# Kernel optimization log

Hardware: AMD Instinct MI355X
Metric: run time of the kernel (lower is better)

Reference implementation:

```python
import jax, jax.numpy as jnp
import numpy as np
import math

SCALE = 64.0
MARGIN = 0.5
THRESH = math.cos(math.pi - MARGIN)          # cos(pi - m)
MM = math.sin(math.pi - MARGIN) * MARGIN     # sin(pi - m) * m
N, D, C = 512, 512, 100000


def setup_inputs() -> dict:
    key = jax.random.key(0)
    k1, k2, k3 = jax.random.split(key, 3)
    x = jax.random.normal(k1, (N, D), dtype=jnp.float32)
    label = jax.random.randint(k2, (N,), 0, C, dtype=jnp.int64)
    # reset_parameters: uniform(-stdv, stdv), stdv = 1/sqrt(in_features)
    stdv = 1.0 / math.sqrt(D)
    weight = jax.random.uniform(k3, (C, D), dtype=jnp.float32, minval=-stdv, maxval=stdv)
    return {"input": x, "label": label, "weight": weight}


def reference(input, label, weight):
    # row-wise L2 normalize features and class weights
    ex = input / jnp.linalg.norm(input, axis=1, keepdims=True)
    ew = weight / jnp.linalg.norm(weight, axis=1, keepdims=True)
    cos = jnp.einsum("nd,cd->nc", ex, ew)               # [N, C]
    rows = jnp.arange(cos.shape[0])
    cos_l = cos[rows, label]                              # cos at the label column
    cond = cos_l > THRESH                                 # easy-margin condition per row
    onehot = (jnp.arange(cos.shape[1])[None, :] == label[:, None])
    a = jnp.where(onehot & cond[:, None], MARGIN, 0.0).astype(cos.dtype)
    b = jnp.where(onehot & (~cond[:, None]), -MM, 0.0).astype(cos.dtype)
    # clamp slightly inside [-1,1] to guard acos against fp roundoff
    cos_c = jnp.clip(cos, -1.0 + 1e-7, 1.0 - 1e-7)
    logits = SCALE * (jnp.cos(jnp.arccos(cos_c) + a) + b)
    return logits
```

## Files before the change

kernel.cpp:

```cpp
#include <hip/hip_runtime.h>
#include <hip/hip_bf16.h>
#include <stdint.h>


#define NROWS 512
#define DDIM 512
#define NCLS 100000
#define NCLS_PAD 100096

typedef __attribute__((ext_vector_type(8))) short bf16x8;
typedef __attribute__((ext_vector_type(4))) float f32x4;

__device__ __forceinline__ unsigned short f2bf(float x) {
    union { float f; uint32_t u; } c; c.f = x;
    uint32_t r = (c.u + 0x7FFFu + ((c.u >> 16) & 1u)) >> 16;
    return (unsigned short)r;
}

__device__ __forceinline__ void g2lds16(const void* g, void* l) {
    __builtin_amdgcn_global_load_lds(
        (const __attribute__((address_space(1))) void*)g,
        (__attribute__((address_space(3))) void*)l, 16, 0, 0);
}

__global__ __launch_bounds__(256)
void rownorm_all(const float* __restrict__ x, const float* __restrict__ w,
                 unsigned short* __restrict__ Abf, unsigned short* __restrict__ Wbf) {
    const int wv   = threadIdx.x >> 6;
    const int lane = threadIdx.x & 63;

    const float* in;
    unsigned short* orow;
    int validRows, row;
    if (blockIdx.x < 128) {
        row = blockIdx.x * 4 + wv;
        in = x; orow = Abf + (size_t)row * DDIM; validRows = NROWS;
    } else {
        row = (blockIdx.x - 128) * 4 + wv;
        in = w; orow = Wbf + (size_t)row * DDIM; validRows = NCLS;
    }

    if (row >= validRows) {
        ushort4 z = {0, 0, 0, 0};
        *(ushort4*)(orow + lane * 4) = z;
        *(ushort4*)(orow + 256 + lane * 4) = z;
        return;
    }

    const float4* p = (const float4*)(in + (size_t)row * DDIM);
    float4 v0 = p[lane];
    float4 v1 = p[64 + lane];

    float ss = v0.x*v0.x + v0.y*v0.y + v0.z*v0.z + v0.w*v0.w
             + v1.x*v1.x + v1.y*v1.y + v1.z*v1.z + v1.w*v1.w;
    #pragma unroll
    for (int off = 32; off > 0; off >>= 1) ss += __shfl_xor(ss, off);
    const float r = rsqrtf(ss);

    ushort4 o0, o1;
    o0.x = f2bf(v0.x * r); o0.y = f2bf(v0.y * r);
    o0.z = f2bf(v0.z * r); o0.w = f2bf(v0.w * r);
    o1.x = f2bf(v1.x * r); o1.y = f2bf(v1.y * r);
    o1.z = f2bf(v1.z * r); o1.w = f2bf(v1.w * r);
    *(ushort4*)(orow + lane * 4) = o0;
    *(ushort4*)(orow + 256 + lane * 4) = o1;
}

__global__ __launch_bounds__(256)
void arcface_gemm(const unsigned short* __restrict__ A,
                  const unsigned short* __restrict__ B,
                  float* __restrict__ out) {
    __shared__ unsigned short As[128 * 32];
    __shared__ unsigned short Bs[128 * 32];

    const int bid = blockIdx.x;
    int panel, slot;
    if (bid < 3104) { panel = (bid >> 5) * 8 + (bid & 7); slot = (bid >> 3) & 3; }
    else            { int l = bid - 3104; panel = 776 + l % 6; slot = l / 6; }
    const int rowBase = slot * 128;
    const int colBase = panel * 128;

    const int t    = threadIdx.x;
    const int lane = t & 63;
    const int wid  = t >> 6;
    const int wr   = wid >> 1;
    const int wc   = wid & 1;

    f32x4 acc[4][4] = {};

    const unsigned short* gA = A + (size_t)(rowBase + (t >> 2)) * DDIM + ((t & 3) << 3);
    const unsigned short* gB = B + (size_t)(colBase + (t >> 2)) * DDIM + ((t & 3) << 3);

    const int kg = (lane >> 4) << 3;
    const int fr = lane & 15;

    for (int kt = 0; kt < DDIM; kt += 32) {
        __syncthreads();
        g2lds16(gA + kt,             &As[t * 8]);
        g2lds16(gA + kt + 64 * DDIM, &As[2048 + t * 8]);
        g2lds16(gB + kt,             &Bs[t * 8]);
        g2lds16(gB + kt + 64 * DDIM, &Bs[2048 + t * 8]);
        __syncthreads();

        bf16x8 a[4], b[4];
        #pragma unroll
        for (int m = 0; m < 4; ++m)
            a[m] = *(const bf16x8*)&As[(wr * 64 + m * 16 + fr) * 32 + kg];
        #pragma unroll
        for (int n = 0; n < 4; ++n)
            b[n] = *(const bf16x8*)&Bs[(wc * 64 + n * 16 + fr) * 32 + kg];

        #pragma unroll
        for (int m = 0; m < 4; ++m)
            #pragma unroll
            for (int n = 0; n < 4; ++n)
                acc[m][n] = __builtin_amdgcn_mfma_f32_16x16x32_bf16(
                    a[m], b[n], acc[m][n], 0, 0, 0);
    }

    const float lo = -1.0f + 1e-7f, hi = 1.0f - 1e-7f;
    #pragma unroll
    for (int m = 0; m < 4; ++m) {
        const int r = rowBase + wr * 64 + m * 16 + ((lane >> 4) << 2);
        #pragma unroll
        for (int n = 0; n < 4; ++n) {
            const int c = colBase + wc * 64 + n * 16 + fr;
            if (c < NCLS) {
                #pragma unroll
                for (int i = 0; i < 4; ++i) {
                    float v = acc[m][n][i];
                    v = fminf(fmaxf(v, lo), hi);
                    out[(size_t)(r + i) * NCLS + c] = 64.0f * v;
                }
            }
        }
    }
}

__global__ void arcface_fixup(const int* __restrict__ label, float* __restrict__ out) {
    const int n = blockIdx.x * 64 + threadIdx.x;
    if (n >= NROWS) return;
    const int c = label[n];
    const size_t idx = (size_t)n * NCLS + c;
    const float t = out[idx] * 0.015625f;
    const float COSM = 0.8775825618903728f;
    const float SINM = 0.479425538604203f;
    const float MM   = 0.2397127693021015f;
    const float THRESH = -0.8775825618903728f;
    float r;
    if (t > THRESH) {
        r = t * COSM - sqrtf(fmaxf(1.0f - t * t, 0.0f)) * SINM;
    } else {
        r = t - MM;
    }
    out[idx] = 64.0f * r;
}

extern "C" void kernel_launch(void* const* d_in, const int* in_sizes, int n_in,
                              void* d_out, int out_size, void* d_ws, size_t ws_size,
                              hipStream_t stream) {
    const float* x     = (const float*)d_in[0];
    const int*   label = (const int*)d_in[1];
    const float* w     = (const float*)d_in[2];
    float* out = (float*)d_out;

    unsigned short* Abf = (unsigned short*)d_ws;
    unsigned short* Wbf = (unsigned short*)d_ws + (size_t)NROWS * DDIM;

    rownorm_all<<<128 + NCLS_PAD / 4, 256, 0, stream>>>(x, w, Abf, Wbf);

    arcface_gemm<<<3128, 256, 0, stream>>>(Abf, Wbf, out);

    arcface_fixup<<<(NROWS + 63) / 64, 64, 0, stream>>>(label, out);
}
```

Baseline: 429.4 us.

## Fuse weight normalization and margin fixup into double-buffered GEMM

```diff
diff --git a/kernel.cpp b/kernel.cpp
--- a/kernel.cpp
+++ b/kernel.cpp
@@ -6,9 +6,9 @@
 #define NROWS 512
 #define DDIM 512
 #define NCLS 100000
-#define NCLS_PAD 100096
 
 typedef __attribute__((ext_vector_type(8))) short bf16x8;
+typedef __attribute__((ext_vector_type(8))) unsigned short u16x8;
 typedef __attribute__((ext_vector_type(4))) float f32x4;
 
 __device__ __forceinline__ unsigned short f2bf(float x) {
@@ -24,28 +24,9 @@
 }
 
 __global__ __launch_bounds__(256)
-void rownorm_all(const float* __restrict__ x, const float* __restrict__ w,
-                 unsigned short* __restrict__ Abf, unsigned short* __restrict__ Wbf) {
-    const int wv   = threadIdx.x >> 6;
+void rownorm_x(const float* __restrict__ in, unsigned short* __restrict__ out) {
+    const int row  = blockIdx.x * 4 + (threadIdx.x >> 6);
     const int lane = threadIdx.x & 63;
-
-    const float* in;
-    unsigned short* orow;
-    int validRows, row;
-    if (blockIdx.x < 128) {
-        row = blockIdx.x * 4 + wv;
-        in = x; orow = Abf + (size_t)row * DDIM; validRows = NROWS;
-    } else {
-        row = (blockIdx.x - 128) * 4 + wv;
-        in = w; orow = Wbf + (size_t)row * DDIM; validRows = NCLS;
-    }
-
-    if (row >= validRows) {
-        ushort4 z = {0, 0, 0, 0};
-        *(ushort4*)(orow + lane * 4) = z;
-        *(ushort4*)(orow + 256 + lane * 4) = z;
-        return;
-    }
 
     const float4* p = (const float4*)(in + (size_t)row * DDIM);
     float4 v0 = p[lane];
@@ -57,6 +38,7 @@
     for (int off = 32; off > 0; off >>= 1) ss += __shfl_xor(ss, off);
     const float r = rsqrtf(ss);
 
+    unsigned short* orow = out + (size_t)row * DDIM;
     ushort4 o0, o1;
     o0.x = f2bf(v0.x * r); o0.y = f2bf(v0.y * r);
     o0.z = f2bf(v0.z * r); o0.w = f2bf(v0.w * r);
@@ -67,11 +49,14 @@
 }
 
 __global__ __launch_bounds__(256)
-void arcface_gemm(const unsigned short* __restrict__ A,
-                  const unsigned short* __restrict__ B,
-                  float* __restrict__ out) {
-    __shared__ unsigned short As[128 * 32];
-    __shared__ unsigned short Bs[128 * 32];
+void arcface_gemm_fused(const unsigned short* __restrict__ A,
+                        const float* __restrict__ W,
+                        const int* __restrict__ labels,
+                        float* __restrict__ out) {
+    __shared__ unsigned short As[2][128 * 32];
+    __shared__ unsigned short Bs[2][128 * 40];
+    __shared__ float ssp[128];
+    __shared__ int   lab_s[128];
 
     const int bid = blockIdx.x;
     int panel, slot;
@@ -85,30 +70,78 @@
     const int wid  = t >> 6;
     const int wr   = wid >> 1;
     const int wc   = wid & 1;
-
+    const int kg   = (lane >> 4) << 3;
+    const int fr   = lane & 15;
+
+    if (t < 128) lab_s[t] = labels[rowBase + t];
+
+    const int brow = t >> 1;
+    const int kc   = (t & 1) << 4;
+    const int cls  = colBase + brow;
+    const bool bv  = cls < NCLS;
+    const float* gB = W + (size_t)(bv ? cls : 0) * DDIM + kc;
+    unsigned short* wB[2] = { &Bs[0][brow * 40 + kc], &Bs[1][brow * 40 + kc] };
+
+    const unsigned short* gA = A + (size_t)(rowBase + (t >> 2)) * DDIM + ((t & 3) << 3);
+
+    float ss = 0.f;
     f32x4 acc[4][4] = {};
 
-    const unsigned short* gA = A + (size_t)(rowBase + (t >> 2)) * DDIM + ((t & 3) << 3);
-    const unsigned short* gB = B + (size_t)(colBase + (t >> 2)) * DDIM + ((t & 3) << 3);
-
-    const int kg = (lane >> 4) << 3;
-    const int fr = lane & 15;
-
-    for (int kt = 0; kt < DDIM; kt += 32) {
-        __syncthreads();
-        g2lds16(gA + kt,             &As[t * 8]);
-        g2lds16(gA + kt + 64 * DDIM, &As[2048 + t * 8]);
-        g2lds16(gB + kt,             &Bs[t * 8]);
-        g2lds16(gB + kt + 64 * DDIM, &Bs[2048 + t * 8]);
-        __syncthreads();
+    float4 p0, p1, p2, p3;
+    g2lds16(gA,             &As[0][t * 8]);
+    g2lds16(gA + 64 * DDIM, &As[0][2048 + t * 8]);
+    if (bv) {
+        p0 = *(const float4*)(gB + 0);  p1 = *(const float4*)(gB + 4);
+        p2 = *(const float4*)(gB + 8);  p3 = *(const float4*)(gB + 12);
+    } else {
+        p0 = float4{0,0,0,0}; p1 = p0; p2 = p0; p3 = p0;
+    }
+
+    #pragma unroll
+    for (int tt = 0; tt < 16; ++tt) {
+        const int cur = tt & 1;
+
+        __builtin_amdgcn_s_barrier();
+        __builtin_amdgcn_sched_barrier(0);
+        asm volatile("s_waitcnt vmcnt(0)" ::: "memory");
+        __builtin_amdgcn_sched_barrier(0);
+
+        ss += p0.x*p0.x + p0.y*p0.y + p0.z*p0.z + p0.w*p0.w;
+        ss += p1.x*p1.x + p1.y*p1.y + p1.z*p1.z + p1.w*p1.w;
+        ss += p2.x*p2.x + p2.y*p2.y + p2.z*p2.z + p2.w*p2.w;
+        ss += p3.x*p3.x + p3.y*p3.y + p3.z*p3.z + p3.w*p3.w;
+        u16x8 o0, o1;
+        o0[0]=f2bf(p0.x); o0[1]=f2bf(p0.y); o0[2]=f2bf(p0.z); o0[3]=f2bf(p0.w);
+        o0[4]=f2bf(p1.x); o0[5]=f2bf(p1.y); o0[6]=f2bf(p1.z); o0[7]=f2bf(p1.w);
+        o1[0]=f2bf(p2.x); o1[1]=f2bf(p2.y); o1[2]=f2bf(p2.z); o1[3]=f2bf(p2.w);
+        o1[4]=f2bf(p3.x); o1[5]=f2bf(p3.y); o1[6]=f2bf(p3.z); o1[7]=f2bf(p3.w);
+        *(u16x8*)(wB[cur])     = o0;
+        *(u16x8*)(wB[cur] + 8) = o1;
+
+        if (tt < 15) {
+            const int kt = (tt + 1) * 32;
+            g2lds16(gA + kt,             &As[cur ^ 1][t * 8]);
+            g2lds16(gA + kt + 64 * DDIM, &As[cur ^ 1][2048 + t * 8]);
+            if (bv) {
+                p0 = *(const float4*)(gB + kt + 0);
+                p1 = *(const float4*)(gB + kt + 4);
+                p2 = *(const float4*)(gB + kt + 8);
+                p3 = *(const float4*)(gB + kt + 12);
+            }
+        }
+
+        asm volatile("s_waitcnt lgkmcnt(0)" ::: "memory");
+        __builtin_amdgcn_sched_barrier(0);
+        __builtin_amdgcn_s_barrier();
+        __builtin_amdgcn_sched_barrier(0);
 
         bf16x8 a[4], b[4];
         #pragma unroll
         for (int m = 0; m < 4; ++m)
-            a[m] = *(const bf16x8*)&As[(wr * 64 + m * 16 + fr) * 32 + kg];
+            a[m] = *(const bf16x8*)&As[cur][(wr * 64 + m * 16 + fr) * 32 + kg];
         #pragma unroll
         for (int n = 0; n < 4; ++n)
-            b[n] = *(const bf16x8*)&Bs[(wc * 64 + n * 16 + fr) * 32 + kg];
+            b[n] = *(const bf16x8*)&Bs[cur][(wc * 64 + n * 16 + fr) * 40 + kg];
 
         #pragma unroll
         for (int m = 0; m < 4; ++m)
@@ -118,42 +151,43 @@
                     a[m], b[n], acc[m][n], 0, 0, 0);
     }
 
+    float sst = ss + __shfl_xor(ss, 1);
+    if ((t & 1) == 0) ssp[t >> 1] = sst;
+    __syncthreads();
+
     const float lo = -1.0f + 1e-7f, hi = 1.0f - 1e-7f;
+    const float COSM = 0.8775825618903728f;
+    const float SINM = 0.479425538604203f;
+    const float MM   = 0.2397127693021015f;
+    const float THR  = -0.8775825618903728f;
+
+    float rn[4];
+    #pragma unroll
+    for (int n = 0; n < 4; ++n)
+        rn[n] = rsqrtf(ssp[wc * 64 + n * 16 + fr]);
+
     #pragma unroll
     for (int m = 0; m < 4; ++m) {
-        const int r = rowBase + wr * 64 + m * 16 + ((lane >> 4) << 2);
+        const int rloc = wr * 64 + m * 16 + ((lane >> 4) << 2);
         #pragma unroll
         for (int n = 0; n < 4; ++n) {
             const int c = colBase + wc * 64 + n * 16 + fr;
             if (c < NCLS) {
                 #pragma unroll
                 for (int i = 0; i < 4; ++i) {
-                    float v = acc[m][n][i];
-                    v = fminf(fmaxf(v, lo), hi);
-                    out[(size_t)(r + i) * NCLS + c] = 64.0f * v;
+                    const float raw = acc[m][n][i] * rn[n];
+                    const float tc  = fminf(fmaxf(raw, lo), hi);
+                    float val = tc;
+                    if (lab_s[rloc + i] == c) {
+                        val = (raw > THR)
+                            ? tc * COSM - sqrtf(fmaxf(1.0f - tc * tc, 0.0f)) * SINM
+                            : tc - MM;
+                    }
+                    out[(size_t)(rowBase + rloc + i) * NCLS + c] = 64.0f * val;
                 }
             }
         }
     }
-}
-
-__global__ void arcface_fixup(const int* __restrict__ label, float* __restrict__ out) {
-    const int n = blockIdx.x * 64 + threadIdx.x;
-    if (n >= NROWS) return;
-    const int c = label[n];
-    const size_t idx = (size_t)n * NCLS + c;
-    const float t = out[idx] * 0.015625f;
-    const float COSM = 0.8775825618903728f;
-    const float SINM = 0.479425538604203f;
-    const float MM   = 0.2397127693021015f;
-    const float THRESH = -0.8775825618903728f;
-    float r;
-    if (t > THRESH) {
-        r = t * COSM - sqrtf(fmaxf(1.0f - t * t, 0.0f)) * SINM;
-    } else {
-        r = t - MM;
-    }
-    out[idx] = 64.0f * r;
 }
 
 extern "C" void kernel_launch(void* const* d_in, const int* in_sizes, int n_in,
@@ -165,11 +199,8 @@
     float* out = (float*)d_out;
 
     unsigned short* Abf = (unsigned short*)d_ws;
-    unsigned short* Wbf = (unsigned short*)d_ws + (size_t)NROWS * DDIM;
-
-    rownorm_all<<<128 + NCLS_PAD / 4, 256, 0, stream>>>(x, w, Abf, Wbf);
-
-    arcface_gemm<<<3128, 256, 0, stream>>>(Abf, Wbf, out);
-
-    arcface_fixup<<<(NROWS + 63) / 64, 64, 0, stream>>>(label, out);
-}
+
+    rownorm_x<<<NROWS / 4, 256, 0, stream>>>(x, Abf);
+
+    arcface_gemm_fused<<<3128, 256, 0, stream>>>(Abf, w, label, out);
+}
```

After: 455.6 us. 6.1% more time.
